# Kernel tuning notes

Measured on AMD Instinct MI355X. Metric: run time of the kernel, lower is better.

Reference implementation:

```python
import jax, jax.numpy as jnp
import numpy as np

N, E = 50000, 800000          # nodes, edges
F_IN, H, C = 32, 64, 7        # input feats, hidden, classes
EPS = 1e-5                    # BatchNorm eps


def setup_inputs() -> dict:
    key = jax.random.key(0)
    ks = jax.random.split(key, 16)
    inp = {
        "x": jax.random.normal(ks[0], (N, F_IN), jnp.float32),
        "edge_index": jax.random.randint(ks[1], (2, E), 0, N),
        "edge_attr": jax.random.uniform(ks[2], (E, 1), jnp.float32),
    }

    def conv_params(k, cin, cout, i):
        k1, k2 = jax.random.split(k)
        s = 1.0 / np.sqrt(cin)
        inp[f"W{i}"] = jax.random.uniform(k1, (2, cin, cout), jnp.float32, -s, s)  # spline kernel weights
        inp[f"R{i}"] = jax.random.uniform(k2, (cin, cout), jnp.float32, -s, s)     # root weight
        inp[f"B{i}"] = jnp.zeros((cout,), jnp.float32)

    conv_params(ks[3], F_IN, H, 0)
    conv_params(ks[4], H, H, 1)
    conv_params(ks[5], H, C, 2)
    for i in range(2):  # BatchNorm (eval mode: running stats)
        inp[f"G{i}"] = jnp.ones((H,), jnp.float32)
        inp[f"BE{i}"] = jnp.zeros((H,), jnp.float32)
        inp[f"RM{i}"] = 0.1 * jax.random.normal(ks[6 + 2 * i], (H,), jnp.float32)
        inp[f"RV{i}"] = jax.random.uniform(ks[7 + 2 * i], (H,), jnp.float32, 0.5, 1.5)
    return inp


def spline_conv(x, src, dst, u, W, R, B):
    # dim=1, kernel_size=2, degree=1 open B-spline:
    # basis = (1-u, u) with weight indices (0, 1) for u in [0,1).
    basis = jnp.stack([1.0 - u, u], axis=1)               # [E, 2]
    msg = jnp.einsum('ec,ek,kco->eo', x[src], basis, W)    # gather + basis-weighted linear
    agg = jax.ops.segment_sum(msg, dst, num_segments=N)    # scatter-add
    deg = jax.ops.segment_sum(jnp.ones((src.shape[0],), x.dtype), dst, num_segments=N)
    agg = agg / jnp.maximum(deg, 1.0)[:, None]             # aggr='mean' (default)
    return agg + x @ R + B                                 # root weight + bias


def batch_norm(x, g, b, rm, rv):
    return (x - rm) * jax.lax.rsqrt(rv + EPS) * g + b


def reference(x, edge_index, edge_attr,
              W0, R0, B0, W1, R1, B1, W2, R2, B2,
              G0, BE0, RM0, RV0, G1, BE1, RM1, RV1):
    src, dst = edge_index[0], edge_index[1]
    u = edge_attr[:, 0]
    h = spline_conv(x, src, dst, u, W0, R0, B0)
    h = jax.nn.elu(batch_norm(h, G0, BE0, RM0, RV0))
    h = spline_conv(h, src, dst, u, W1, R1, B1)
    h = jax.nn.elu(batch_norm(h, G1, BE1, RM1, RV1))
    h = spline_conv(h, src, dst, u, W2, R2, B2)
    return jax.nn.log_softmax(h, axis=1)
```

## Files before the change

### kernel.cpp

```cpp
#include <hip/hip_runtime.h>
#include <hip/hip_fp16.h>
#include <math.h>

#define NN 50000
#define NE 800000
#define EPSV 1e-5f
#define BSHIFT 7
#define BSIZE 128
#define NB 391
#define CAP 2560

typedef _Float16 h2f   __attribute__((ext_vector_type(2)));
typedef _Float16 f16x8 __attribute__((ext_vector_type(8)));
typedef float    f32x4 __attribute__((ext_vector_type(4)));

__global__ __launch_bounds__(64) void prep_all_kernel(
        const float* __restrict__ W0, const float* __restrict__ R0,
        const float* __restrict__ W1, const float* __restrict__ R1,
        const float* __restrict__ W2, const float* __restrict__ R2,
        const float* __restrict__ B0, const float* __restrict__ B1,
        const float* __restrict__ G0, const float* __restrict__ BE0,
        const float* __restrict__ RM0, const float* __restrict__ RV0,
        const float* __restrict__ G1, const float* __restrict__ BE1,
        const float* __restrict__ RM1, const float* __restrict__ RV1,
        __half* __restrict__ Bf0, __half* __restrict__ Bf1, __half* __restrict__ Bf7,
        float* __restrict__ bn0, float* __restrict__ bn1,
        int* __restrict__ bcursor) {
    int lane = threadIdx.x;
    int bid = blockIdx.x;
    int c = lane & 15;
    int kbase = ((lane >> 4) << 3);
    _Float16 vals[8];
    if (bid < 12) {
        int ks = bid >> 2, nt = bid & 3;
        int n = nt * 16 + c;
#pragma unroll
        for (int j = 0; j < 8; ++j) {
            int kg = ks * 32 + kbase + j;
            float v = (kg < 64) ? W0[(kg & 1) * 2048 + (kg >> 1) * 64 + n]
                                : R0[(kg - 64) * 64 + n];
            vals[j] = (_Float16)v;
        }
        *reinterpret_cast<f16x8*>(Bf0 + ((size_t)(bid * 64 + lane)) * 8) =
            *reinterpret_cast<f16x8*>(vals);
    } else if (bid < 36) {
        int t = bid - 12;
        int ks = t >> 2, nt = t & 3;
        int n = nt * 16 + c;
#pragma unroll
        for (int j = 0; j < 8; ++j) {
            int kg = ks * 32 + kbase + j;
            float v = (kg < 128) ? W1[(kg & 1) * 4096 + (kg >> 1) * 64 + n]
                                 : R1[(kg - 128) * 64 + n];
            vals[j] = (_Float16)v;
        }
        *reinterpret_cast<f16x8*>(Bf1 + ((size_t)(t * 64 + lane)) * 8) =
            *reinterpret_cast<f16x8*>(vals);
    } else if (bid < 40) {
        int ksnt = bid - 36;
        int ks = ksnt >> 1, nt = ksnt & 1;
#pragma unroll
        for (int j = 0; j < 8; ++j) {
            int k = ks * 32 + kbase + j;
            float v = 0.f;
            if (nt == 0) {
                if (c < 7)                 v = W2[k * 7 + c];
                else if (c >= 8 && c < 15) v = W2[448 + k * 7 + (c - 8)];
            } else {
                if (c < 7)                 v = R2[k * 7 + c];
            }
            vals[j] = (_Float16)v;
        }
        *reinterpret_cast<f16x8*>(Bf7 + ((size_t)(ksnt * 64 + lane)) * 8) =
            *reinterpret_cast<f16x8*>(vals);
    } else if (bid == 40) {
        float s = G0[lane] * rsqrtf(RV0[lane] + EPSV);
        bn0[lane] = s;
        bn0[64 + lane] = B0[lane] * s + BE0[lane] - RM0[lane] * s;
    } else if (bid == 41) {
        float s = G1[lane] * rsqrtf(RV1[lane] + EPSV);
        bn1[lane] = s;
        bn1[64 + lane] = B1[lane] * s + BE1[lane] - RM1[lane] * s;
    } else {
        int b = (bid - 42) * 64 + lane;
        if (b < NB) bcursor[b] = b * CAP;
    }
}

__global__ __launch_bounds__(256) void binB_xh_kernel(
        const int* __restrict__ src, const int* __restrict__ dst,
        const float* __restrict__ attr, int* __restrict__ bcursor,
        unsigned* __restrict__ es1su, unsigned char* __restrict__ es1dl, int E,
        const float* __restrict__ x, __half* __restrict__ xh) {
    __shared__ int hist[NB];
    __shared__ int base[NB];
    if (blockIdx.x >= NB) {
        int t = (blockIdx.x - NB) * 256 + threadIdx.x;
        size_t idx = (size_t)t * 8;
        if (idx < (size_t)NN * 32) {
            float4 f0 = *reinterpret_cast<const float4*>(x + idx);
            float4 f1 = *reinterpret_cast<const float4*>(x + idx + 4);
            _Float16 v[8] = {(_Float16)f0.x, (_Float16)f0.y, (_Float16)f0.z, (_Float16)f0.w,
                             (_Float16)f1.x, (_Float16)f1.y, (_Float16)f1.z, (_Float16)f1.w};
            *reinterpret_cast<f16x8*>(xh + idx) = *reinterpret_cast<f16x8*>(v);
        }
        return;
    }
    for (int i = threadIdx.x; i < NB; i += blockDim.x) hist[i] = 0;
    __syncthreads();
    const int chunk = (E + NB - 1) / NB;
    int e0 = blockIdx.x * chunk;
    int e1 = e0 + chunk; if (e1 > E) e1 = E;
    unsigned su[8]; unsigned char dlv[8]; short bv[8];
#pragma unroll
    for (int j = 0; j < 8; ++j) {
        int e = e0 + threadIdx.x + j * 256;
        if (e < e1) {
            int d = dst[e];
            int b = d >> BSHIFT;
            __half uh = __float2half_rn(attr[e]);
            su[j]  = ((unsigned)src[e] << 16) | (unsigned)__half_as_ushort(uh);
            dlv[j] = (unsigned char)(d & (BSIZE - 1));
            bv[j]  = (short)b;
            atomicAdd(&hist[b], 1);
        }
    }
    __syncthreads();
    for (int i = threadIdx.x; i < NB; i += blockDim.x) {
        int cnt = hist[i];
        base[i] = cnt ? atomicAdd(&bcursor[i], cnt) : 0;
        hist[i] = 0;
    }
    __syncthreads();
#pragma unroll
    for (int j = 0; j < 8; ++j) {
        int e = e0 + threadIdx.x + j * 256;
        if (e < e1) {
            int b = bv[j];
            int slot = base[b] + atomicAdd(&hist[b], 1);
            es1su[slot] = su[j];
            es1dl[slot] = dlv[j];
        }
    }
}

__global__ __launch_bounds__(256) void placeC_kernel(const int* __restrict__ bcursor,
                                                     const unsigned* __restrict__ es1su,
                                                     const unsigned char* __restrict__ es1dl,
                                                     int2* __restrict__ rowrange,
                                                     uint2* __restrict__ es8) {
    __shared__ int hist[BSIZE];
    __shared__ int stmp[BSIZE];
    __shared__ int cur[BSIZE];
    int b = blockIdx.x;
    int t = threadIdx.x;
    int bs = b * CAP;
    int be = bcursor[b];
    if (t < BSIZE) hist[t] = 0;
    __syncthreads();
    unsigned su[10]; unsigned char dlv[10];
#pragma unroll
    for (int j = 0; j < 10; ++j) {
        int i = bs + t + j * 256;
        if (i < be) {
            su[j]  = es1su[i];
            dlv[j] = es1dl[i];
            atomicAdd(&hist[dlv[j]], 1);
        }
    }
    __syncthreads();
    if (t < BSIZE) {
        int v = hist[t];
        int incl = v;
#pragma unroll
        for (int o = 1; o < 64; o <<= 1) {
            int nv = __shfl_up(incl, o, 64);
            if ((t & 63) >= o) incl += nv;
        }
        stmp[t] = incl;
    }
    __syncthreads();
    if (t < BSIZE) {
        int excl = stmp[t] - hist[t] + ((t >= 64) ? stmp[63] : 0);
        cur[t] = excl;
        int node = b * BSIZE + t;
        if (node < NN) {
            int2 rr; rr.x = bs + excl; rr.y = bs + excl + hist[t];
            rowrange[node] = rr;
        }
    }
    __syncthreads();
#pragma unroll
    for (int j = 0; j < 10; ++j) {
        int i = bs + t + j * 256;
        if (i < be) {
            unsigned r = su[j];
            int dl = dlv[j];
            int slot = bs + atomicAdd(&cur[dl], 1);
            __half uh = __ushort_as_half((unsigned short)(r & 0xffffu));
            __half2 p = __halves2half2(__hsub(__ushort_as_half((unsigned short)0x3C00u), uh), uh);
            uint2 rec;
            rec.x = r >> 16;
            rec.y = *reinterpret_cast<unsigned*>(&p);
            es8[slot] = rec;
        }
    }
}

__global__ __launch_bounds__(256) void gatherS32_kernel(const int2* __restrict__ rowrange,
                                                        const uint2* __restrict__ es8,
                                                        const __half* __restrict__ xh,
                                                        __half* __restrict__ S, int n_nodes) {
    int n = (blockIdx.x * blockDim.x + threadIdx.x) >> 6;
    int lane = threadIdx.x & 63;
    if (n >= n_nodes) return;
    int2 rr = rowrange[n];
    int beg = __builtin_amdgcn_readfirstlane(rr.x);
    int end = __builtin_amdgcn_readfirstlane(rr.y);
    int c = lane & 31;
    const __half* xb = xh + c;
    float a0 = 0.f, a1 = 0.f, a2 = 0.f, a3 = 0.f;
    float b0 = 0.f, b1 = 0.f, b2 = 0.f, b3 = 0.f;
    int i = beg + (lane >> 5);
    for (; i + 6 < end; i += 8) {
        uint2 q0 = es8[i];
        uint2 q1 = es8[i + 2];
        uint2 q2 = es8[i + 4];
        uint2 q3 = es8[i + 6];
        float x0 = __half2float(xb[(size_t)q0.x << 5]);
        float x1 = __half2float(xb[(size_t)q1.x << 5]);
        float x2 = __half2float(xb[(size_t)q2.x << 5]);
        float x3 = __half2float(xb[(size_t)q3.x << 5]);
        __half2 u0 = __builtin_bit_cast(__half2, q0.y);
        __half2 u1 = __builtin_bit_cast(__half2, q1.y);
        __half2 u2 = __builtin_bit_cast(__half2, q2.y);
        __half2 u3 = __builtin_bit_cast(__half2, q3.y);
        a0 = fmaf(__low2float(u0), x0, a0); b0 = fmaf(__high2float(u0), x0, b0);
        a1 = fmaf(__low2float(u1), x1, a1); b1 = fmaf(__high2float(u1), x1, b1);
        a2 = fmaf(__low2float(u2), x2, a2); b2 = fmaf(__high2float(u2), x2, b2);
        a3 = fmaf(__low2float(u3), x3, a3); b3 = fmaf(__high2float(u3), x3, b3);
    }
    for (; i < end; i += 2) {
        uint2 q = es8[i];
        float xv = __half2float(xb[(size_t)q.x << 5]);
        __half2 u = __builtin_bit_cast(__half2, q.y);
        a0 = fmaf(__low2float(u), xv, a0); b0 = fmaf(__high2float(u), xv, b0);
    }
    float a = (a0 + a1) + (a2 + a3);
    float b = (b0 + b1) + (b2 + b3);
    a += __shfl_xor(a, 32);
    b += __shfl_xor(b, 32);
    float degv = (float)(end - beg);
    if (degv < 1.f) degv = 1.f;
    float inv = 1.f / degv;
    if (lane < 32) {
        reinterpret_cast<__half2*>(S + (size_t)n * 64)[c] = __floats2half2_rn(a * inv, b * inv);
    }
}

__global__ __launch_bounds__(256) void gatherS64_kernel(const int2* __restrict__ rowrange,
                                                        const uint2* __restrict__ es8,
                                                        const __half* __restrict__ ht,
                                                        __half* __restrict__ S, int n_nodes) {
    int n = (blockIdx.x * blockDim.x + threadIdx.x) >> 6;
    int lane = threadIdx.x & 63;
    if (n >= n_nodes) return;
    int2 rr = rowrange[n];
    int beg = __builtin_amdgcn_readfirstlane(rr.x);
    int end = __builtin_amdgcn_readfirstlane(rr.y);
    const __half* xb = ht + lane;
    float a0 = 0.f, a1 = 0.f, a2 = 0.f, a3 = 0.f;
    float b0 = 0.f, b1 = 0.f, b2 = 0.f, b3 = 0.f;
    int i = beg;
    if (i < end && (i & 1)) {
        uint2 q = es8[i];
        float xv = __half2float(xb[(size_t)q.x << 6]);
        __half2 u = __builtin_bit_cast(__half2, q.y);
        a0 = fmaf(__low2float(u), xv, a0); b0 = fmaf(__high2float(u), xv, b0);
        ++i;
    }
    for (; i + 7 < end; i += 8) {
        uint4 p0 = *reinterpret_cast<const uint4*>(es8 + i);
        uint4 p1 = *reinterpret_cast<const uint4*>(es8 + i + 2);
        uint4 p2 = *reinterpret_cast<const uint4*>(es8 + i + 4);
        uint4 p3 = *reinterpret_cast<const uint4*>(es8 + i + 6);
        float x0 = __half2float(xb[(size_t)p0.x << 6]);
        float x1 = __half2float(xb[(size_t)p0.z << 6]);
        float x2 = __half2float(xb[(size_t)p1.x << 6]);
        float x3 = __half2float(xb[(size_t)p1.z << 6]);
        float x4 = __half2float(xb[(size_t)p2.x << 6]);
        float x5 = __half2float(xb[(size_t)p2.z << 6]);
        float x6 = __half2float(xb[(size_t)p3.x << 6]);
        float x7 = __half2float(xb[(size_t)p3.z << 6]);
        __half2 u0 = __builtin_bit_cast(__half2, p0.y);
        __half2 u1 = __builtin_bit_cast(__half2, p0.w);
        __half2 u2 = __builtin_bit_cast(__half2, p1.y);
        __half2 u3 = __builtin_bit_cast(__half2, p1.w);
        __half2 u4 = __builtin_bit_cast(__half2, p2.y);
        __half2 u5 = __builtin_bit_cast(__half2, p2.w);
        __half2 u6 = __builtin_bit_cast(__half2, p3.y);
        __half2 u7 = __builtin_bit_cast(__half2, p3.w);
        a0 = fmaf(__low2float(u0), x0, a0); b0 = fmaf(__high2float(u0), x0, b0);
        a1 = fmaf(__low2float(u1), x1, a1); b1 = fmaf(__high2float(u1), x1, b1);
        a2 = fmaf(__low2float(u2), x2, a2); b2 = fmaf(__high2float(u2), x2, b2);
        a3 = fmaf(__low2float(u3), x3, a3); b3 = fmaf(__high2float(u3), x3, b3);
        a0 = fmaf(__low2float(u4), x4, a0); b0 = fmaf(__high2float(u4), x4, b0);
        a1 = fmaf(__low2float(u5), x5, a1); b1 = fmaf(__high2float(u5), x5, b1);
        a2 = fmaf(__low2float(u6), x6, a2); b2 = fmaf(__high2float(u6), x6, b2);
        a3 = fmaf(__low2float(u7), x7, a3); b3 = fmaf(__high2float(u7), x7, b3);
    }
    for (; i + 1 < end; i += 2) {
        uint4 p = *reinterpret_cast<const uint4*>(es8 + i);
        float x0 = __half2float(xb[(size_t)p.x << 6]);
        float x1 = __half2float(xb[(size_t)p.z << 6]);
        __half2 u0 = __builtin_bit_cast(__half2, p.y);
        __half2 u1 = __builtin_bit_cast(__half2, p.w);
        a0 = fmaf(__low2float(u0), x0, a0); b0 = fmaf(__high2float(u0), x0, b0);
        a1 = fmaf(__low2float(u1), x1, a1); b1 = fmaf(__high2float(u1), x1, b1);
    }
    if (i < end) {
        uint2 q = es8[i];
        float xv = __half2float(xb[(size_t)q.x << 6]);
        __half2 u = __builtin_bit_cast(__half2, q.y);
        a0 = fmaf(__low2float(u), xv, a0); b0 = fmaf(__high2float(u), xv, b0);
    }
    float a = (a0 + a1) + (a2 + a3);
    float b = (b0 + b1) + (b2 + b3);
    float degv = (float)(end - beg);
    if (degv < 1.f) degv = 1.f;
    float inv = 1.f / degv;
    reinterpret_cast<__half2*>(S + (size_t)n * 128)[lane] = __floats2half2_rn(a * inv, b * inv);
}

__global__ __launch_bounds__(256) void gemmL0_kernel(const __half* __restrict__ S,
                                                     const __half* __restrict__ xh,
                                                     const __half* __restrict__ Bf0,
                                                     const float* __restrict__ bn,
                                                     __half* __restrict__ hout, int n_nodes) {
    const int lane = threadIdx.x & 63;
    const int wid  = threadIdx.x >> 6;
    int m0 = (blockIdx.x * 4 + wid) * 16;
    if (m0 >= n_nodes) return;
    f32x4 acc[4];
#pragma unroll
    for (int i = 0; i < 4; ++i) acc[i] = (f32x4){0.f, 0.f, 0.f, 0.f};
    const int arow = m0 + (lane & 15);
    const int koff = ((lane >> 4) << 3);
    const f16x8* bf = reinterpret_cast<const f16x8*>(Bf0);
    const _Float16* sp = (const _Float16*)S  + (size_t)arow * 64 + koff;
    const _Float16* xp = (const _Float16*)xh + (size_t)arow * 32 + koff;
    f16x8 a0 = *reinterpret_cast<const f16x8*>(sp);
    f16x8 a1 = *reinterpret_cast<const f16x8*>(sp + 32);
    f16x8 a2 = *reinterpret_cast<const f16x8*>(xp);
#pragma unroll
    for (int nt = 0; nt < 4; ++nt)
        acc[nt] = __builtin_amdgcn_mfma_f32_16x16x32_f16(a0, bf[nt * 64 + lane], acc[nt], 0, 0, 0);
#pragma unroll
    for (int nt = 0; nt < 4; ++nt)
        acc[nt] = __builtin_amdgcn_mfma_f32_16x16x32_f16(a1, bf[(4 + nt) * 64 + lane], acc[nt], 0, 0, 0);
#pragma unroll
    for (int nt = 0; nt < 4; ++nt)
        acc[nt] = __builtin_amdgcn_mfma_f32_16x16x32_f16(a2, bf[(8 + nt) * 64 + lane], acc[nt], 0, 0, 0);
    const int c_lo  = lane & 15;
    const int rbase = ((lane >> 4) << 2);
#pragma unroll
    for (int nt = 0; nt < 4; ++nt) {
        int cc = nt * 16 + c_lo;
        float sc = bn[cc], sh = bn[64 + cc];
#pragma unroll
        for (int r = 0; r < 4; ++r) {
            int row = m0 + rbase + r;
            float v = acc[nt][r] * sc + sh;
            v = v > 0.f ? v : expm1f(v);
            hout[(size_t)row * 64 + cc] = __float2half(v);
        }
    }
}

__global__ __launch_bounds__(256) void gemmL1_kernel(const __half* __restrict__ S,
                                                     const __half* __restrict__ hin,
                                                     const __half* __restrict__ Bf1,
                                                     const float* __restrict__ bn,
                                                     __half* __restrict__ hout, int n_nodes) {
    const int lane = threadIdx.x & 63;
    const int wid  = threadIdx.x >> 6;
    int m0 = (blockIdx.x * 4 + wid) * 16;
    if (m0 >= n_nodes) return;
    f32x4 acc[4];
#pragma unroll
    for (int i = 0; i < 4; ++i) acc[i] = (f32x4){0.f, 0.f, 0.f, 0.f};
    const int arow = m0 + (lane & 15);
    const int koff = ((lane >> 4) << 3);
    const f16x8* bf = reinterpret_cast<const f16x8*>(Bf1);
    const _Float16* sp = (const _Float16*)S   + (size_t)arow * 128 + koff;
    const _Float16* hp = (const _Float16*)hin + (size_t)arow * 64  + koff;
#pragma unroll
    for (int ks = 0; ks < 6; ++ks) {
        f16x8 av = (ks < 4) ? *reinterpret_cast<const f16x8*>(sp + ks * 32)
                            : *reinterpret_cast<const f16x8*>(hp + (ks - 4) * 32);
#pragma unroll
        for (int nt = 0; nt < 4; ++nt)
            acc[nt] = __builtin_amdgcn_mfma_f32_16x16x32_f16(av, bf[(ks * 4 + nt) * 64 + lane], acc[nt], 0, 0, 0);
    }
    const int c_lo  = lane & 15;
    const int rbase = ((lane >> 4) << 2);
#pragma unroll
    for (int nt = 0; nt < 4; ++nt) {
        int cc = nt * 16 + c_lo;
        float sc = bn[cc], sh = bn[64 + cc];
#pragma unroll
        for (int r = 0; r < 4; ++r) {
            int row = m0 + rbase + r;
            float v = acc[nt][r] * sc + sh;
            v = v > 0.f ? v : expm1f(v);
            hout[(size_t)row * 64 + cc] = __float2half(v);
        }
    }
}

__global__ __launch_bounds__(256) void gemm7_kernel(const __half* __restrict__ h,
                               const __half* __restrict__ Bf7,
                               const float* __restrict__ Bb,
                               __half* __restrict__ Yab7H,
                               float* __restrict__ Z7,
                               int n_nodes) {
    const int lane = threadIdx.x & 63;
    const int wid  = threadIdx.x >> 6;
    int m0 = (blockIdx.x * 4 + wid) * 16;
    if (m0 >= n_nodes) return;

    f32x4 acc[2];
    acc[0] = (f32x4){0.f, 0.f, 0.f, 0.f};
    acc[1] = (f32x4){0.f, 0.f, 0.f, 0.f};
    const int arow = m0 + (lane & 15);
    const int koff = ((lane >> 4) << 3);
    const f16x8* bf = reinterpret_cast<const f16x8*>(Bf7);
#pragma unroll
    for (int ks = 0; ks < 2; ++ks) {
        f16x8 av = *reinterpret_cast<const f16x8*>(
            (const _Float16*)h + (size_t)arow * 64 + ks * 32 + koff);
#pragma unroll
        for (int nt = 0; nt < 2; ++nt) {
            f16x8 bv = bf[(ks * 2 + nt) * 64 + lane];
            acc[nt] = __builtin_amdgcn_mfma_f32_16x16x32_f16(av, bv, acc[nt], 0, 0, 0);
        }
    }
    const int c_lo  = lane & 15;
    const int rbase = ((lane >> 4) << 2);
#pragma unroll
    for (int r = 0; r < 4; ++r) {
        int row = m0 + rbase + r;
        if (c_lo < 7) {
            Yab7H[(size_t)row * 14 + 2 * c_lo] = __float2half(acc[0][r]);
            Z7[(size_t)row * 7 + c_lo] = acc[1][r] + Bb[c_lo];
        } else if (c_lo >= 8 && c_lo < 15) {
            Yab7H[(size_t)row * 14 + 2 * (c_lo - 8) + 1] = __float2half(acc[0][r]);
        }
    }
}

__global__ void gather7_final_kernel(const int2* __restrict__ rowrange,
                                     const uint2* __restrict__ es8,
                                     const __half2* __restrict__ Yab7H,
                                     const float* __restrict__ Z7,
                                     float* __restrict__ out, int n_nodes) {
    int t = blockIdx.x * blockDim.x + threadIdx.x;
    int n = t >> 3;
    int c = t & 7;
    if (n >= n_nodes) return;
    int2 rr = rowrange[n];
    int beg = rr.x, end = rr.y;
    float acc0 = 0.f, acc1 = 0.f, acc2 = 0.f, acc3 = 0.f;
    if (c < 7) {
        int i = beg;
        for (; i + 3 < end; i += 4) {
            uint2 q0 = es8[i];
            uint2 q1 = es8[i + 1];
            uint2 q2 = es8[i + 2];
            uint2 q3 = es8[i + 3];
            __half2 v0 = Yab7H[(size_t)q0.x * 7 + c];
            __half2 v1 = Yab7H[(size_t)q1.x * 7 + c];
            __half2 v2 = Yab7H[(size_t)q2.x * 7 + c];
            __half2 v3 = Yab7H[(size_t)q3.x * 7 + c];
            acc0 = __builtin_amdgcn_fdot2(__builtin_bit_cast(h2f, v0), __builtin_bit_cast(h2f, q0.y), acc0, false);
            acc1 = __builtin_amdgcn_fdot2(__builtin_bit_cast(h2f, v1), __builtin_bit_cast(h2f, q1.y), acc1, false);
            acc2 = __builtin_amdgcn_fdot2(__builtin_bit_cast(h2f, v2), __builtin_bit_cast(h2f, q2.y), acc2, false);
            acc3 = __builtin_amdgcn_fdot2(__builtin_bit_cast(h2f, v3), __builtin_bit_cast(h2f, q3.y), acc3, false);
        }
        for (; i < end; ++i) {
            uint2 q = es8[i];
            __half2 v = Yab7H[(size_t)q.x * 7 + c];
            acc0 = __builtin_amdgcn_fdot2(__builtin_bit_cast(h2f, v), __builtin_bit_cast(h2f, q.y), acc0, false);
        }
    }
    float acc = (acc0 + acc1) + (acc2 + acc3);
    float degv = (float)(end - beg);
    if (degv < 1.f) degv = 1.f;
    float v = (c < 7) ? (acc / degv + Z7[n * 7 + c]) : -1e30f;
    float m = v;
#pragma unroll
    for (int o = 1; o < 8; o <<= 1) m = fmaxf(m, __shfl_xor(m, o, 8));
    float ex = (c < 7) ? expf(v - m) : 0.f;
    float ssum = ex;
#pragma unroll
    for (int o = 1; o < 8; o <<= 1) ssum += __shfl_xor(ssum, o, 8);
    if (c < 7) out[n * 7 + c] = v - m - logf(ssum);
}

extern "C" void kernel_launch(void* const* d_in, const int* in_sizes, int n_in,
                              void* d_out, int out_size, void* d_ws, size_t ws_size,
                              hipStream_t stream) {
    const float* x    = (const float*)d_in[0];
    const int*   ei   = (const int*)d_in[1];
    const float* attr = (const float*)d_in[2];
    const float* W0 = (const float*)d_in[3];
    const float* R0 = (const float*)d_in[4];
    const float* B0 = (const float*)d_in[5];
    const float* W1 = (const float*)d_in[6];
    const float* R1 = (const float*)d_in[7];
    const float* B1 = (const float*)d_in[8];
    const float* W2 = (const float*)d_in[9];
    const float* R2 = (const float*)d_in[10];
    const float* B2 = (const float*)d_in[11];
    const float* G0  = (const float*)d_in[12];
    const float* BE0 = (const float*)d_in[13];
    const float* RM0 = (const float*)d_in[14];
    const float* RV0 = (const float*)d_in[15];
    const float* G1  = (const float*)d_in[16];
    const float* BE1 = (const float*)d_in[17];
    const float* RM1 = (const float*)d_in[18];
    const float* RV1 = (const float*)d_in[19];

    const int* src = ei;
    const int* dst = ei + NE;
    float* out = (float*)d_out;

    char* ws = (char*)d_ws;
    size_t off = 0;
    auto alloc = [&](size_t bytes) { char* p = ws + off; off += (bytes + 255) & ~size_t(255); return p; };
    int*           bcursor  = (int*)          alloc(NB * sizeof(int));
    int2*          rowrange = (int2*)         alloc((size_t)NN * sizeof(int2));
    unsigned*      es1su    = (unsigned*)     alloc((size_t)NB * CAP * sizeof(unsigned));
    unsigned char* es1dl    = (unsigned char*)alloc((size_t)NB * CAP * sizeof(unsigned char));
    uint2*         es8      = (uint2*)        alloc((size_t)NB * CAP * sizeof(uint2));
    __half*        Bf0      = (__half*)       alloc((size_t)12 * 64 * 8 * sizeof(__half));
    __half*        Bf1      = (__half*)       alloc((size_t)24 * 64 * 8 * sizeof(__half));
    __half*        Bf7      = (__half*)       alloc((size_t)4 * 64 * 8 * sizeof(__half));
    float*         bn0      = (float*)        alloc(128 * sizeof(float));
    float*         bn1      = (float*)        alloc(128 * sizeof(float));
    __half*        xh       = (__half*)       alloc((size_t)NN * 32 * sizeof(__half));
    __half*        S        = (__half*)       alloc((size_t)NN * 128 * sizeof(__half));
    __half*        h0       = (__half*)       alloc((size_t)NN * 64 * sizeof(__half));
    __half*        h1       = (__half*)       alloc((size_t)NN * 64 * sizeof(__half));
    __half*        Yab7H    = (__half*)       alloc((size_t)NN * 14 * sizeof(__half));
    float*         Z7       = (float*)        alloc((size_t)NN * 7 * sizeof(float));

    const int B = 256;
    const int gM    = ((NN + 15) / 16 + 3) / 4;
    const int gGath = (NN * 64) / (B);
    const int gN8   = (NN * 8 + B - 1) / B;
    const int gConv = ((NN * 32 / 8) + B - 1) / B;
    const int gPrep = 42 + (NB + 63) / 64;

    prep_all_kernel<<<gPrep, 64, 0, stream>>>(W0, R0, W1, R1, W2, R2, B0, B1,
                                              G0, BE0, RM0, RV0, G1, BE1, RM1, RV1,
                                              Bf0, Bf1, Bf7, bn0, bn1, bcursor);

    binB_xh_kernel<<<NB + gConv, B, 0, stream>>>(src, dst, attr, bcursor, es1su, es1dl, NE, x, xh);

    placeC_kernel<<<NB, B, 0, stream>>>(bcursor, es1su, es1dl, rowrange, es8);

    gatherS32_kernel<<<gGath, B, 0, stream>>>(rowrange, es8, xh, S, NN);
    gemmL0_kernel<<<gM, B, 0, stream>>>(S, xh, Bf0, bn0, h0, NN);

    gatherS64_kernel<<<gGath, B, 0, stream>>>(rowrange, es8, h0, S, NN);
    gemmL1_kernel<<<gM, B, 0, stream>>>(S, h0, Bf1, bn1, h1, NN);

    gemm7_kernel<<<gM, B, 0, stream>>>(h1, Bf7, B2, Yab7H, Z7, NN);
    gather7_final_kernel<<<gN8, B, 0, stream>>>(rowrange, es8, (const __half2*)Yab7H, Z7, out, NN);
}
```

Before: 209.3 us.

## Fuse neighbor gathers with MFMA GEMMs via LDS, merge layer-2 projection

Gather-mean aggregation and the following MFMA GEMM are merged into one kernel per layer. Each wave aggregates 16 nodes into swizzled LDS and then feeds that tile straight to the matrix cores, so the global S buffer and its write/read round trip go away. The layer-1 kernel also keeps its post-BN/ELU output in LDS and runs the 7-class projection in place, which drops the h1 buffer and the separate gemm7 launch. In exchange, each wave now handles 16 nodes one after another in the gather phase, which lowers gather parallelism and latency hiding, and LDS use per block goes up.

```diff
diff --git a/kernel.cpp b/kernel.cpp
--- a/kernel.cpp
+++ b/kernel.cpp
@@ -207,160 +207,91 @@
     }
 }
 
-__global__ __launch_bounds__(256) void gatherS32_kernel(const int2* __restrict__ rowrange,
-                                                        const uint2* __restrict__ es8,
-                                                        const __half* __restrict__ xh,
-                                                        __half* __restrict__ S, int n_nodes) {
-    int n = (blockIdx.x * blockDim.x + threadIdx.x) >> 6;
-    int lane = threadIdx.x & 63;
-    if (n >= n_nodes) return;
-    int2 rr = rowrange[n];
-    int beg = __builtin_amdgcn_readfirstlane(rr.x);
-    int end = __builtin_amdgcn_readfirstlane(rr.y);
-    int c = lane & 31;
-    const __half* xb = xh + c;
-    float a0 = 0.f, a1 = 0.f, a2 = 0.f, a3 = 0.f;
-    float b0 = 0.f, b1 = 0.f, b2 = 0.f, b3 = 0.f;
-    int i = beg + (lane >> 5);
-    for (; i + 6 < end; i += 8) {
-        uint2 q0 = es8[i];
-        uint2 q1 = es8[i + 2];
-        uint2 q2 = es8[i + 4];
-        uint2 q3 = es8[i + 6];
-        float x0 = __half2float(xb[(size_t)q0.x << 5]);
-        float x1 = __half2float(xb[(size_t)q1.x << 5]);
-        float x2 = __half2float(xb[(size_t)q2.x << 5]);
-        float x3 = __half2float(xb[(size_t)q3.x << 5]);
-        __half2 u0 = __builtin_bit_cast(__half2, q0.y);
-        __half2 u1 = __builtin_bit_cast(__half2, q1.y);
-        __half2 u2 = __builtin_bit_cast(__half2, q2.y);
-        __half2 u3 = __builtin_bit_cast(__half2, q3.y);
-        a0 = fmaf(__low2float(u0), x0, a0); b0 = fmaf(__high2float(u0), x0, b0);
-        a1 = fmaf(__low2float(u1), x1, a1); b1 = fmaf(__high2float(u1), x1, b1);
-        a2 = fmaf(__low2float(u2), x2, a2); b2 = fmaf(__high2float(u2), x2, b2);
-        a3 = fmaf(__low2float(u3), x3, a3); b3 = fmaf(__high2float(u3), x3, b3);
-    }
-    for (; i < end; i += 2) {
-        uint2 q = es8[i];
-        float xv = __half2float(xb[(size_t)q.x << 5]);
-        __half2 u = __builtin_bit_cast(__half2, q.y);
-        a0 = fmaf(__low2float(u), xv, a0); b0 = fmaf(__high2float(u), xv, b0);
-    }
-    float a = (a0 + a1) + (a2 + a3);
-    float b = (b0 + b1) + (b2 + b3);
-    a += __shfl_xor(a, 32);
-    b += __shfl_xor(b, 32);
-    float degv = (float)(end - beg);
-    if (degv < 1.f) degv = 1.f;
-    float inv = 1.f / degv;
-    if (lane < 32) {
-        reinterpret_cast<__half2*>(S + (size_t)n * 64)[c] = __floats2half2_rn(a * inv, b * inv);
-    }
-}
-
-__global__ __launch_bounds__(256) void gatherS64_kernel(const int2* __restrict__ rowrange,
-                                                        const uint2* __restrict__ es8,
-                                                        const __half* __restrict__ ht,
-                                                        __half* __restrict__ S, int n_nodes) {
-    int n = (blockIdx.x * blockDim.x + threadIdx.x) >> 6;
-    int lane = threadIdx.x & 63;
-    if (n >= n_nodes) return;
-    int2 rr = rowrange[n];
-    int beg = __builtin_amdgcn_readfirstlane(rr.x);
-    int end = __builtin_amdgcn_readfirstlane(rr.y);
-    const __half* xb = ht + lane;
-    float a0 = 0.f, a1 = 0.f, a2 = 0.f, a3 = 0.f;
-    float b0 = 0.f, b1 = 0.f, b2 = 0.f, b3 = 0.f;
-    int i = beg;
-    if (i < end && (i & 1)) {
-        uint2 q = es8[i];
-        float xv = __half2float(xb[(size_t)q.x << 6]);
-        __half2 u = __builtin_bit_cast(__half2, q.y);
-        a0 = fmaf(__low2float(u), xv, a0); b0 = fmaf(__high2float(u), xv, b0);
-        ++i;
-    }
-    for (; i + 7 < end; i += 8) {
-        uint4 p0 = *reinterpret_cast<const uint4*>(es8 + i);
-        uint4 p1 = *reinterpret_cast<const uint4*>(es8 + i + 2);
-        uint4 p2 = *reinterpret_cast<const uint4*>(es8 + i + 4);
-        uint4 p3 = *reinterpret_cast<const uint4*>(es8 + i + 6);
-        float x0 = __half2float(xb[(size_t)p0.x << 6]);
-        float x1 = __half2float(xb[(size_t)p0.z << 6]);
-        float x2 = __half2float(xb[(size_t)p1.x << 6]);
-        float x3 = __half2float(xb[(size_t)p1.z << 6]);
-        float x4 = __half2float(xb[(size_t)p2.x << 6]);
-        float x5 = __half2float(xb[(size_t)p2.z << 6]);
-        float x6 = __half2float(xb[(size_t)p3.x << 6]);
-        float x7 = __half2float(xb[(size_t)p3.z << 6]);
-        __half2 u0 = __builtin_bit_cast(__half2, p0.y);
-        __half2 u1 = __builtin_bit_cast(__half2, p0.w);
-        __half2 u2 = __builtin_bit_cast(__half2, p1.y);
-        __half2 u3 = __builtin_bit_cast(__half2, p1.w);
-        __half2 u4 = __builtin_bit_cast(__half2, p2.y);
-        __half2 u5 = __builtin_bit_cast(__half2, p2.w);
-        __half2 u6 = __builtin_bit_cast(__half2, p3.y);
-        __half2 u7 = __builtin_bit_cast(__half2, p3.w);
-        a0 = fmaf(__low2float(u0), x0, a0); b0 = fmaf(__high2float(u0), x0, b0);
-        a1 = fmaf(__low2float(u1), x1, a1); b1 = fmaf(__high2float(u1), x1, b1);
-        a2 = fmaf(__low2float(u2), x2, a2); b2 = fmaf(__high2float(u2), x2, b2);
-        a3 = fmaf(__low2float(u3), x3, a3); b3 = fmaf(__high2float(u3), x3, b3);
-        a0 = fmaf(__low2float(u4), x4, a0); b0 = fmaf(__high2float(u4), x4, b0);
-        a1 = fmaf(__low2float(u5), x5, a1); b1 = fmaf(__high2float(u5), x5, b1);
-        a2 = fmaf(__low2float(u6), x6, a2); b2 = fmaf(__high2float(u6), x6, b2);
-        a3 = fmaf(__low2float(u7), x7, a3); b3 = fmaf(__high2float(u7), x7, b3);
-    }
-    for (; i + 1 < end; i += 2) {
-        uint4 p = *reinterpret_cast<const uint4*>(es8 + i);
-        float x0 = __half2float(xb[(size_t)p.x << 6]);
-        float x1 = __half2float(xb[(size_t)p.z << 6]);
-        __half2 u0 = __builtin_bit_cast(__half2, p.y);
-        __half2 u1 = __builtin_bit_cast(__half2, p.w);
-        a0 = fmaf(__low2float(u0), x0, a0); b0 = fmaf(__high2float(u0), x0, b0);
-        a1 = fmaf(__low2float(u1), x1, a1); b1 = fmaf(__high2float(u1), x1, b1);
-    }
-    if (i < end) {
-        uint2 q = es8[i];
-        float xv = __half2float(xb[(size_t)q.x << 6]);
-        __half2 u = __builtin_bit_cast(__half2, q.y);
-        a0 = fmaf(__low2float(u), xv, a0); b0 = fmaf(__high2float(u), xv, b0);
-    }
-    float a = (a0 + a1) + (a2 + a3);
-    float b = (b0 + b1) + (b2 + b3);
-    float degv = (float)(end - beg);
-    if (degv < 1.f) degv = 1.f;
-    float inv = 1.f / degv;
-    reinterpret_cast<__half2*>(S + (size_t)n * 128)[lane] = __floats2half2_rn(a * inv, b * inv);
-}
-
-__global__ __launch_bounds__(256) void gemmL0_kernel(const __half* __restrict__ S,
-                                                     const __half* __restrict__ xh,
-                                                     const __half* __restrict__ Bf0,
-                                                     const float* __restrict__ bn,
-                                                     __half* __restrict__ hout, int n_nodes) {
+__global__ __launch_bounds__(256) void fusedL0_kernel(const int2* __restrict__ rowrange,
+                                                      const uint2* __restrict__ es8,
+                                                      const __half* __restrict__ xh,
+                                                      const __half* __restrict__ Bf0,
+                                                      const float* __restrict__ bn,
+                                                      __half* __restrict__ h0, int n_nodes) {
+    __shared__ __align__(16) char lds[64 * 128];
     const int lane = threadIdx.x & 63;
     const int wid  = threadIdx.x >> 6;
-    int m0 = (blockIdx.x * 4 + wid) * 16;
-    if (m0 >= n_nodes) return;
+    const int nbase = blockIdx.x * 64 + wid * 16;
+    if (nbase >= n_nodes) return;
+
+    int2 rr0 = {0, 0};
+    if (lane < 16 && nbase + lane < n_nodes) rr0 = rowrange[nbase + lane];
+
+    const int c = lane & 31;
+    const __half* xb = xh + c;
+#pragma unroll 1
+    for (int k = 0; k < 16; ++k) {
+        int n = nbase + k;
+        if (n >= n_nodes) break;
+        int beg = __shfl(rr0.x, k, 64);
+        int end = __shfl(rr0.y, k, 64);
+        float a0 = 0.f, a1 = 0.f, a2 = 0.f, a3 = 0.f;
+        float b0 = 0.f, b1 = 0.f, b2 = 0.f, b3 = 0.f;
+        int i = beg + (lane >> 5);
+        for (; i + 6 < end; i += 8) {
+            uint2 q0 = es8[i];
+            uint2 q1 = es8[i + 2];
+            uint2 q2 = es8[i + 4];
+            uint2 q3 = es8[i + 6];
+            float x0 = __half2float(xb[(size_t)q0.x << 5]);
+            float x1 = __half2float(xb[(size_t)q1.x << 5]);
+            float x2 = __half2float(xb[(size_t)q2.x << 5]);
+            float x3 = __half2float(xb[(size_t)q3.x << 5]);
+            __half2 u0 = __builtin_bit_cast(__half2, q0.y);
+            __half2 u1 = __builtin_bit_cast(__half2, q1.y);
+            __half2 u2 = __builtin_bit_cast(__half2, q2.y);
+            __half2 u3 = __builtin_bit_cast(__half2, q3.y);
+            a0 = fmaf(__low2float(u0), x0, a0); b0 = fmaf(__high2float(u0), x0, b0);
+            a1 = fmaf(__low2float(u1), x1, a1); b1 = fmaf(__high2float(u1), x1, b1);
+            a2 = fmaf(__low2float(u2), x2, a2); b2 = fmaf(__high2float(u2), x2, b2);
+            a3 = fmaf(__low2float(u3), x3, a3); b3 = fmaf(__high2float(u3), x3, b3);
+        }
+        for (; i < end; i += 2) {
+            uint2 q = es8[i];
+            float xv = __half2float(xb[(size_t)q.x << 5]);
+            __half2 u = __builtin_bit_cast(__half2, q.y);
+            a0 = fmaf(__low2float(u), xv, a0); b0 = fmaf(__high2float(u), xv, b0);
+        }
+        float a = (a0 + a1) + (a2 + a3);
+        float b = (b0 + b1) + (b2 + b3);
+        a += __shfl_xor(a, 32);
+        b += __shfl_xor(b, 32);
+        float degv = (float)(end - beg);
+        if (degv < 1.f) degv = 1.f;
+        float inv = 1.f / degv;
+        if (lane < 32) {
+            int row = wid * 16 + k;
+            int byte = (row * 128 + c * 4) ^ ((row & 7) << 4);
+            *reinterpret_cast<__half2*>(lds + byte) = __floats2half2_rn(a * inv, b * inv);
+        }
+    }
+
+    const int m0 = nbase;
     f32x4 acc[4];
 #pragma unroll
     for (int i = 0; i < 4; ++i) acc[i] = (f32x4){0.f, 0.f, 0.f, 0.f};
+    const int rowl = wid * 16 + (lane & 15);
+    const int g = lane >> 4;
+    const int koff = g << 3;
     const int arow = m0 + (lane & 15);
-    const int koff = ((lane >> 4) << 3);
     const f16x8* bf = reinterpret_cast<const f16x8*>(Bf0);
-    const _Float16* sp = (const _Float16*)S  + (size_t)arow * 64 + koff;
-    const _Float16* xp = (const _Float16*)xh + (size_t)arow * 32 + koff;
-    f16x8 a0 = *reinterpret_cast<const f16x8*>(sp);
-    f16x8 a1 = *reinterpret_cast<const f16x8*>(sp + 32);
-    f16x8 a2 = *reinterpret_cast<const f16x8*>(xp);
+    f16x8 a0v = *reinterpret_cast<const f16x8*>(lds + ((rowl * 128 + g * 16) ^ ((rowl & 7) << 4)));
+    f16x8 a1v = *reinterpret_cast<const f16x8*>(lds + ((rowl * 128 + 64 + g * 16) ^ ((rowl & 7) << 4)));
+    f16x8 a2v = *reinterpret_cast<const f16x8*>((const _Float16*)xh + (size_t)arow * 32 + koff);
 #pragma unroll
     for (int nt = 0; nt < 4; ++nt)
-        acc[nt] = __builtin_amdgcn_mfma_f32_16x16x32_f16(a0, bf[nt * 64 + lane], acc[nt], 0, 0, 0);
+        acc[nt] = __builtin_amdgcn_mfma_f32_16x16x32_f16(a0v, bf[nt * 64 + lane], acc[nt], 0, 0, 0);
 #pragma unroll
     for (int nt = 0; nt < 4; ++nt)
-        acc[nt] = __builtin_amdgcn_mfma_f32_16x16x32_f16(a1, bf[(4 + nt) * 64 + lane], acc[nt], 0, 0, 0);
+        acc[nt] = __builtin_amdgcn_mfma_f32_16x16x32_f16(a1v, bf[(4 + nt) * 64 + lane], acc[nt], 0, 0, 0);
 #pragma unroll
     for (int nt = 0; nt < 4; ++nt)
-        acc[nt] = __builtin_amdgcn_mfma_f32_16x16x32_f16(a2, bf[(8 + nt) * 64 + lane], acc[nt], 0, 0, 0);
+        acc[nt] = __builtin_amdgcn_mfma_f32_16x16x32_f16(a2v, bf[(8 + nt) * 64 + lane], acc[nt], 0, 0, 0);
     const int c_lo  = lane & 15;
     const int rbase = ((lane >> 4) << 2);
 #pragma unroll
@@ -370,34 +301,121 @@
 #pragma unroll
         for (int r = 0; r < 4; ++r) {
             int row = m0 + rbase + r;
-            float v = acc[nt][r] * sc + sh;
-            v = v > 0.f ? v : expm1f(v);
-            hout[(size_t)row * 64 + cc] = __float2half(v);
-        }
-    }
-}
-
-__global__ __launch_bounds__(256) void gemmL1_kernel(const __half* __restrict__ S,
-                                                     const __half* __restrict__ hin,
-                                                     const __half* __restrict__ Bf1,
-                                                     const float* __restrict__ bn,
-                                                     __half* __restrict__ hout, int n_nodes) {
+            if (row < n_nodes) {
+                float v = acc[nt][r] * sc + sh;
+                v = v > 0.f ? v : expm1f(v);
+                h0[(size_t)row * 64 + cc] = __float2half(v);
+            }
+        }
+    }
+}
+
+__global__ __launch_bounds__(256) void fusedL1_kernel(const int2* __restrict__ rowrange,
+                                                      const uint2* __restrict__ es8,
+                                                      const __half* __restrict__ h0,
+                                                      const __half* __restrict__ Bf1,
+                                                      const __half* __restrict__ Bf7,
+                                                      const float* __restrict__ bn,
+                                                      const float* __restrict__ Bb2,
+                                                      __half* __restrict__ Yab7H,
+                                                      float* __restrict__ Z7, int n_nodes) {
+    __shared__ __align__(16) char ldsS[64 * 256];
+    __shared__ __align__(16) char ldsH[64 * 128];
     const int lane = threadIdx.x & 63;
     const int wid  = threadIdx.x >> 6;
-    int m0 = (blockIdx.x * 4 + wid) * 16;
-    if (m0 >= n_nodes) return;
+    const int nbase = blockIdx.x * 64 + wid * 16;
+    if (nbase >= n_nodes) return;
+
+    int2 rr0 = {0, 0};
+    if (lane < 16 && nbase + lane < n_nodes) rr0 = rowrange[nbase + lane];
+
+    const __half* xb = h0 + lane;
+#pragma unroll 1
+    for (int k = 0; k < 16; ++k) {
+        int n = nbase + k;
+        if (n >= n_nodes) break;
+        int beg = __shfl(rr0.x, k, 64);
+        int end = __shfl(rr0.y, k, 64);
+        float a0 = 0.f, a1 = 0.f, a2 = 0.f, a3 = 0.f;
+        float b0 = 0.f, b1 = 0.f, b2 = 0.f, b3 = 0.f;
+        int i = beg;
+        if (i < end && (i & 1)) {
+            uint2 q = es8[i];
+            float xv = __half2float(xb[(size_t)q.x << 6]);
+            __half2 u = __builtin_bit_cast(__half2, q.y);
+            a0 = fmaf(__low2float(u), xv, a0); b0 = fmaf(__high2float(u), xv, b0);
+            ++i;
+        }
+        for (; i + 7 < end; i += 8) {
+            uint4 p0 = *reinterpret_cast<const uint4*>(es8 + i);
+            uint4 p1 = *reinterpret_cast<const uint4*>(es8 + i + 2);
+            uint4 p2 = *reinterpret_cast<const uint4*>(es8 + i + 4);
+            uint4 p3 = *reinterpret_cast<const uint4*>(es8 + i + 6);
+            float x0 = __half2float(xb[(size_t)p0.x << 6]);
+            float x1 = __half2float(xb[(size_t)p0.z << 6]);
+            float x2 = __half2float(xb[(size_t)p1.x << 6]);
+            float x3 = __half2float(xb[(size_t)p1.z << 6]);
+            float x4 = __half2float(xb[(size_t)p2.x << 6]);
+            float x5 = __half2float(xb[(size_t)p2.z << 6]);
+            float x6 = __half2float(xb[(size_t)p3.x << 6]);
+            float x7 = __half2float(xb[(size_t)p3.z << 6]);
+            __half2 u0 = __builtin_bit_cast(__half2, p0.y);
+            __half2 u1 = __builtin_bit_cast(__half2, p0.w);
+            __half2 u2 = __builtin_bit_cast(__half2, p1.y);
+            __half2 u3 = __builtin_bit_cast(__half2, p1.w);
+            __half2 u4 = __builtin_bit_cast(__half2, p2.y);
+            __half2 u5 = __builtin_bit_cast(__half2, p2.w);
+            __half2 u6 = __builtin_bit_cast(__half2, p3.y);
+            __half2 u7 = __builtin_bit_cast(__half2, p3.w);
+            a0 = fmaf(__low2float(u0), x0, a0); b0 = fmaf(__high2float(u0), x0, b0);
+            a1 = fmaf(__low2float(u1), x1, a1); b1 = fmaf(__high2float(u1), x1, b1);
+            a2 = fmaf(__low2float(u2), x2, a2); b2 = fmaf(__high2float(u2), x2, b2);
+            a3 = fmaf(__low2float(u3), x3, a3); b3 = fmaf(__high2float(u3), x3, b3);
+            a0 = fmaf(__low2float(u4), x4, a0); b0 = fmaf(__high2float(u4), x4, b0);
+            a1 = fmaf(__low2float(u5), x5, a1); b1 = fmaf(__high2float(u5), x5, b1);
+            a2 = fmaf(__low2float(u6), x6, a2); b2 = fmaf(__high2float(u6), x6, b2);
+            a3 = fmaf(__low2float(u7), x7, a3); b3 = fmaf(__high2float(u7), x7, b3);
+        }
+        for (; i + 1 < end; i += 2) {
+            uint4 p = *reinterpret_cast<const uint4*>(es8 + i);
+            float x0 = __half2float(xb[(size_t)p.x << 6]);
+            float x1 = __half2float(xb[(size_t)p.z << 6]);
+            __half2 u0 = __builtin_bit_cast(__half2, p.y);
+            __half2 u1 = __builtin_bit_cast(__half2, p.w);
+            a0 = fmaf(__low2float(u0), x0, a0); b0 = fmaf(__high2float(u0), x0, b0);
+            a1 = fmaf(__low2float(u1), x1, a1); b1 = fmaf(__high2float(u1), x1, b1);
+        }
+        if (i < end) {
+            uint2 q = es8[i];
+            float xv = __half2float(xb[(size_t)q.x << 6]);
+            __half2 u = __builtin_bit_cast(__half2, q.y);
+            a0 = fmaf(__low2float(u), xv, a0); b0 = fmaf(__high2float(u), xv, b0);
+        }
+        float a = (a0 + a1) + (a2 + a3);
+        float b = (b0 + b1) + (b2 + b3);
+        float degv = (float)(end - beg);
+        if (degv < 1.f) degv = 1.f;
+        float inv = 1.f / degv;
+        int row = wid * 16 + k;
+        int byte = (row * 256 + lane * 4) ^ ((row & 7) << 4);
+        *reinterpret_cast<__half2*>(ldsS + byte) = __floats2half2_rn(a * inv, b * inv);
+    }
+
+    const int m0 = nbase;
     f32x4 acc[4];
 #pragma unroll
     for (int i = 0; i < 4; ++i) acc[i] = (f32x4){0.f, 0.f, 0.f, 0.f};
+    const int rowl = wid * 16 + (lane & 15);
+    const int g = lane >> 4;
+    const int koff = g << 3;
     const int arow = m0 + (lane & 15);
-    const int koff = ((lane >> 4) << 3);
+    const int swz = (rowl & 7) << 4;
     const f16x8* bf = reinterpret_cast<const f16x8*>(Bf1);
-    const _Float16* sp = (const _Float16*)S   + (size_t)arow * 128 + koff;
-    const _Float16* hp = (const _Float16*)hin + (size_t)arow * 64  + koff;
 #pragma unroll
     for (int ks = 0; ks < 6; ++ks) {
-        f16x8 av = (ks < 4) ? *reinterpret_cast<const f16x8*>(sp + ks * 32)
-                            : *reinterpret_cast<const f16x8*>(hp + (ks - 4) * 32);
+        f16x8 av;
+        if (ks < 4) av = *reinterpret_cast<const f16x8*>(ldsS + ((rowl * 256 + ks * 64 + g * 16) ^ swz));
+        else        av = *reinterpret_cast<const f16x8*>((const _Float16*)h0 + (size_t)arow * 64 + (ks - 4) * 32 + koff);
 #pragma unroll
         for (int nt = 0; nt < 4; ++nt)
             acc[nt] = __builtin_amdgcn_mfma_f32_16x16x32_f16(av, bf[(ks * 4 + nt) * 64 + lane], acc[nt], 0, 0, 0);
@@ -410,51 +428,34 @@
         float sc = bn[cc], sh = bn[64 + cc];
 #pragma unroll
         for (int r = 0; r < 4; ++r) {
-            int row = m0 + rbase + r;
             float v = acc[nt][r] * sc + sh;
             v = v > 0.f ? v : expm1f(v);
-            hout[(size_t)row * 64 + cc] = __float2half(v);
-        }
-    }
-}
-
-__global__ __launch_bounds__(256) void gemm7_kernel(const __half* __restrict__ h,
-                               const __half* __restrict__ Bf7,
-                               const float* __restrict__ Bb,
-                               __half* __restrict__ Yab7H,
-                               float* __restrict__ Z7,
-                               int n_nodes) {
-    const int lane = threadIdx.x & 63;
-    const int wid  = threadIdx.x >> 6;
-    int m0 = (blockIdx.x * 4 + wid) * 16;
-    if (m0 >= n_nodes) return;
-
-    f32x4 acc[2];
-    acc[0] = (f32x4){0.f, 0.f, 0.f, 0.f};
-    acc[1] = (f32x4){0.f, 0.f, 0.f, 0.f};
-    const int arow = m0 + (lane & 15);
-    const int koff = ((lane >> 4) << 3);
-    const f16x8* bf = reinterpret_cast<const f16x8*>(Bf7);
+            int rl = wid * 16 + rbase + r;
+            *reinterpret_cast<__half*>(ldsH + ((rl * 128 + cc * 2) ^ ((rl & 7) << 4))) = __float2half(v);
+        }
+    }
+
+    f32x4 acc7[2];
+    acc7[0] = (f32x4){0.f, 0.f, 0.f, 0.f};
+    acc7[1] = (f32x4){0.f, 0.f, 0.f, 0.f};
+    const f16x8* bf7 = reinterpret_cast<const f16x8*>(Bf7);
 #pragma unroll
     for (int ks = 0; ks < 2; ++ks) {
-        f16x8 av = *reinterpret_cast<const f16x8*>(
-            (const _Float16*)h + (size_t)arow * 64 + ks * 32 + koff);
-#pragma unroll
-        for (int nt = 0; nt < 2; ++nt) {
-            f16x8 bv = bf[(ks * 2 + nt) * 64 + lane];
-            acc[nt] = __builtin_amdgcn_mfma_f32_16x16x32_f16(av, bv, acc[nt], 0, 0, 0);
-        }
-    }
-    const int c_lo  = lane & 15;
-    const int rbase = ((lane >> 4) << 2);
+        f16x8 av = *reinterpret_cast<const f16x8*>(ldsH + ((rowl * 128 + ks * 64 + g * 16) ^ swz));
+#pragma unroll
+        for (int nt = 0; nt < 2; ++nt)
+            acc7[nt] = __builtin_amdgcn_mfma_f32_16x16x32_f16(av, bf7[(ks * 2 + nt) * 64 + lane], acc7[nt], 0, 0, 0);
+    }
 #pragma unroll
     for (int r = 0; r < 4; ++r) {
         int row = m0 + rbase + r;
-        if (c_lo < 7) {
-            Yab7H[(size_t)row * 14 + 2 * c_lo] = __float2half(acc[0][r]);
-            Z7[(size_t)row * 7 + c_lo] = acc[1][r] + Bb[c_lo];
-        } else if (c_lo >= 8 && c_lo < 15) {
-            Yab7H[(size_t)row * 14 + 2 * (c_lo - 8) + 1] = __float2half(acc[0][r]);
+        if (row < n_nodes) {
+            if (c_lo < 7) {
+                Yab7H[(size_t)row * 14 + 2 * c_lo] = __float2half(acc7[0][r]);
+                Z7[(size_t)row * 7 + c_lo] = acc7[1][r] + Bb2[c_lo];
+            } else if (c_lo >= 8 && c_lo < 15) {
+                Yab7H[(size_t)row * 14 + 2 * (c_lo - 8) + 1] = __float2half(acc7[0][r]);
+            }
         }
     }
 }
@@ -548,16 +549,13 @@
     __half*        Bf7      = (__half*)       alloc((size_t)4 * 64 * 8 * sizeof(__half));
     float*         bn0      = (float*)        alloc(128 * sizeof(float));
     float*         bn1      = (float*)        alloc(128 * sizeof(float));
-    __half*        xh       = (__half*)       alloc((size_t)NN * 32 * sizeof(__half));
-    __half*        S        = (__half*)       alloc((size_t)NN * 128 * sizeof(__half));
-    __half*        h0       = (__half*)       alloc((size_t)NN * 64 * sizeof(__half));
-    __half*        h1       = (__half*)       alloc((size_t)NN * 64 * sizeof(__half));
+    __half*        xh       = (__half*)       alloc((size_t)(NN + 64) * 32 * sizeof(__half));
+    __half*        h0       = (__half*)       alloc((size_t)(NN + 64) * 64 * sizeof(__half));
     __half*        Yab7H    = (__half*)       alloc((size_t)NN * 14 * sizeof(__half));
     float*         Z7       = (float*)        alloc((size_t)NN * 7 * sizeof(float));
 
     const int B = 256;
-    const int gM    = ((NN + 15) / 16 + 3) / 4;
-    const int gGath = (NN * 64) / (B);
+    const int gFuse = (NN + 63) / 64;
     const int gN8   = (NN * 8 + B - 1) / B;
     const int gConv = ((NN * 32 / 8) + B - 1) / B;
     const int gPrep = 42 + (NB + 63) / 64;
@@ -570,12 +568,9 @@
 
     placeC_kernel<<<NB, B, 0, stream>>>(bcursor, es1su, es1dl, rowrange, es8);
 
-    gatherS32_kernel<<<gGath, B, 0, stream>>>(rowrange, es8, xh, S, NN);
-    gemmL0_kernel<<<gM, B, 0, stream>>>(S, xh, Bf0, bn0, h0, NN);
-
-    gatherS64_kernel<<<gGath, B, 0, stream>>>(rowrange, es8, h0, S, NN);
-    gemmL1_kernel<<<gM, B, 0, stream>>>(S, h0, Bf1, bn1, h1, NN);
-
-    gemm7_kernel<<<gM, B, 0, stream>>>(h1, Bf7, B2, Yab7H, Z7, NN);
+    fusedL0_kernel<<<gFuse, B, 0, stream>>>(rowrange, es8, xh, Bf0, bn0, h0, NN);
+
+    fusedL1_kernel<<<gFuse, B, 0, stream>>>(rowrange, es8, h0, Bf1, Bf7, bn1, B2, Yab7H, Z7, NN);
+
     gather7_final_kernel<<<gN8, B, 0, stream>>>(rowrange, es8, (const __half2*)Yab7H, Z7, out, NN);
 }
```

New measurement: 240.7 us. 1.15x slower.
